# Kernel optimization log

Hardware: AMD Instinct MI355X
Metric: run time of the kernel (lower is better)

Reference implementation:

```python
import jax, jax.numpy as jnp
import numpy as np

B, S, D, NH, NKV, HD = 1, 2048, 4096, 32, 8, 128
SCALE = HD ** -0.5


def setup_inputs() -> dict:
    key = jax.random.key(0)
    ks = jax.random.split(key, 5)
    sd = D ** -0.5
    x = jax.random.normal(ks[0], (B, S, D), jnp.float32)
    Wq = jax.random.normal(ks[1], (D, NH * HD), jnp.float32) * sd
    Wk = jax.random.normal(ks[2], (D, NKV * HD), jnp.float32) * sd
    Wv = jax.random.normal(ks[3], (D, NKV * HD), jnp.float32) * sd
    Wo = jax.random.normal(ks[4], (NH * HD, D), jnp.float32) * sd
    # real rotary tables (rotate-half convention), shape [S, HD]
    inv_freq = 1.0 / (10000.0 ** (np.arange(0, HD, 2, dtype=np.float64) / HD))
    ang = np.outer(np.arange(S, dtype=np.float64), inv_freq)  # [S, HD//2]
    emb = np.concatenate([ang, ang], axis=-1)  # [S, HD]
    cos = jnp.asarray(np.cos(emb), jnp.float32)
    sin = jnp.asarray(np.sin(emb), jnp.float32)
    return dict(x=x, Wq=Wq, Wk=Wk, Wv=Wv, Wo=Wo, cos=cos, sin=sin)


def _rope(t, cos, sin):
    # t: [B,S,H,HD]; cos/sin: [S,HD]
    c = cos[None, :, None, :]
    s = sin[None, :, None, :]
    t1, t2 = jnp.split(t, 2, axis=-1)
    rot = jnp.concatenate([-t2, t1], axis=-1)
    return t * c + rot * s


def _to_i8(t):
    # per-vector absmax quantization over last dim
    scale = 127.0 / jnp.clip(jnp.max(jnp.abs(t), axis=-1, keepdims=True), 1e-5, None)
    q = jnp.clip(jnp.round(t * scale), -128.0, 127.0).astype(jnp.int8)
    return q, scale


def reference(x, Wq, Wk, Wv, Wo, cos, sin):
    q = (x @ Wq).reshape(B, S, NH, HD)
    k = (x @ Wk).reshape(B, S, NKV, HD)
    v = (x @ Wv).reshape(B, S, NKV, HD)
    q = _rope(q, cos, sin)
    k = _rope(k, cos, sin)
    q_i8, q_s = _to_i8(q)          # [B,S,NH,HD], [B,S,NH,1]
    k_i8, k_s = _to_i8(k)          # [B,S,NKV,HD], [B,S,NKV,1]
    rep = NH // NKV                # GQA expansion
    k_i8 = jnp.repeat(k_i8, rep, axis=2)
    k_s = jnp.repeat(k_s, rep, axis=2)
    v = jnp.repeat(v, rep, axis=2)
    # int8 QK^T accumulated in int32 (exact), then per-vector dequant
    scores = jnp.einsum('bshd,bthd->bhst', q_i8, k_i8,
                        preferred_element_type=jnp.int32).astype(jnp.float32)
    q_st = jnp.transpose(q_s, (0, 2, 1, 3))            # [B,NH,S,1]
    k_st = jnp.transpose(k_s, (0, 2, 3, 1))            # [B,NH,1,S]
    scores = scores * (SCALE / (q_st * k_st))
    # causal mask (seq > 1, no cache so total == S)
    mask = jnp.triu(jnp.full((S, S), -jnp.inf, jnp.float32), k=1)
    scores = scores + mask
    attn = jax.nn.softmax(scores, axis=-1)             # [B,NH,S,S]
    out = jnp.einsum('bhst,bthd->bshd', attn, v).reshape(B, S, NH * HD)
    return out @ Wo
```

## Files before the change

kernel.cpp:

```cpp
#include <hip/hip_runtime.h>
#include <hip/hip_bf16.h>

#define S_LEN 2048
#define DMODEL 4096
#define NH 32
#define NKV 8
#define HD 128
#define NQKV 6144
#define ATT_SCALE_L2E 0.1275175213528852f

typedef __bf16 bf16x8 __attribute__((ext_vector_type(8)));
typedef __bf16 bf16x4 __attribute__((ext_vector_type(4)));
typedef float f32x4 __attribute__((ext_vector_type(4)));

__device__ __forceinline__ unsigned short f2b(float f) {
  union { float f; unsigned u; } a; a.f = f;
  unsigned u = a.u;
  return (unsigned short)((u + 0x7FFFu + ((u >> 16) & 1u)) >> 16);
}
__device__ __forceinline__ float b2f(unsigned short u) {
  union { unsigned u; float f; } a; a.u = (unsigned)u << 16; return a.f;
}

__device__ __forceinline__ void gl16(const unsigned short* g, unsigned short* l) {
  __builtin_amdgcn_global_load_lds(
      (const __attribute__((address_space(1))) unsigned int*)g,
      (__attribute__((address_space(3))) unsigned int*)l, 16, 0, 0);
}

__global__ __launch_bounds__(256) void k_cvt_x(const float* __restrict__ x,
                                               unsigned short* __restrict__ xb) {
  int i = blockIdx.x * 256 + threadIdx.x;
  float4 v = ((const float4*)x)[i];
  ushort4 o;
  o.x = f2b(v.x); o.y = f2b(v.y); o.z = f2b(v.z); o.w = f2b(v.w);
  ((ushort4*)xb)[i] = o;
}

__global__ __launch_bounds__(256) void k_transpose(const float* __restrict__ W,
                                                   unsigned short* __restrict__ Wt,
                                                   int K, int N) {
  __shared__ float tile[64][65];
  int k0 = blockIdx.x * 64, n0 = blockIdx.y * 64;
  int tx = threadIdx.x & 31, ty = threadIdx.x >> 5;
#pragma unroll
  for (int i = 0; i < 8; ++i) {
    int k = ty + i * 8;
    const float* src = W + (size_t)(k0 + k) * N + n0;
    tile[k][tx] = src[tx];
    tile[k][tx + 32] = src[tx + 32];
  }
  __syncthreads();
  int kq = threadIdx.x & 15, nb = threadIdx.x >> 4;
#pragma unroll
  for (int i = 0; i < 4; ++i) {
    int n = nb + i * 16;
    ushort4 o;
    o.x = f2b(tile[kq * 4 + 0][n]);
    o.y = f2b(tile[kq * 4 + 1][n]);
    o.z = f2b(tile[kq * 4 + 2][n]);
    o.w = f2b(tile[kq * 4 + 3][n]);
    *(ushort4*)&Wt[(size_t)(n0 + n) * K + k0 + kq * 4] = o;
  }
}

__global__ __launch_bounds__(256) void k_vt(const unsigned short* __restrict__ v_bf,
                                            unsigned short* __restrict__ v_t) {
  __shared__ unsigned short tile[64][65];
  int s0 = blockIdx.x * 64, d0 = blockIdx.y * 64, kvh = blockIdx.z;
  int tx = threadIdx.x & 63, ty = threadIdx.x >> 6;
#pragma unroll
  for (int i = 0; i < 16; ++i) {
    int s = ty + i * 4;
    tile[s][tx] = v_bf[((size_t)(s0 + s) * NKV + kvh) * HD + d0 + tx];
  }
  __syncthreads();
#pragma unroll
  for (int i = 0; i < 16; ++i) {
    int d = ty + i * 4;
    v_t[((size_t)kvh * HD + d0 + d) * S_LEN + s0 + tx] = tile[tx][d];
  }
}

template <int FN, bool BF16OUT>
__global__ __launch_bounds__(512, 4) void k_g128(const unsigned short* __restrict__ A,
                                                 const unsigned short* __restrict__ B,
                                                 void* __restrict__ Cv,
                                                 int M, int N, int K) {
  extern __shared__ __align__(16) unsigned short smem[];
  char* Sc = (char*)smem;
  const int tid = threadIdx.x;
  const int wvid = tid >> 6, l = tid & 63;
  const int wm = wvid >> 2, wn = wvid & 3;
  const int l15 = l & 15, l4 = l >> 4;

  const int cpx = gridDim.x >> 3;
  const int swz = (blockIdx.x & 7) * cpx + (blockIdx.x >> 3);
  const int mtiles = M >> 7;
  const int m0 = (swz % mtiles) * 128;
  const int n0 = (swz / mtiles) * (FN * 64);

  const int NT = K >> 6;

  const int rsw = (l15 & 7) << 4;
  const int a_base = (wm * 64 + l15) * 128;
  const int b_base = (wn * FN * 16 + l15) * 128;
  const int c0 = (l4 * 16) ^ rsw;
  const int c1 = (64 + l4 * 16) ^ rsw;

  const int srow = l >> 3;
  const int st_k8 = (l & 7) ^ (srow & 7);

  auto stA = [&](int tt) {
    if (tt >= NT) return;
    const unsigned short* g = A + (size_t)(m0 + wvid * 8 + srow) * K + tt * 64 + st_k8 * 8;
    char* lb = Sc + (tt & 1) * 16384 + wvid * 1024;
#pragma unroll
    for (int j = 0; j < 2; ++j)
      gl16(g + (size_t)(j * 64) * K, (unsigned short*)(lb + j * 8192));
  };
  auto stB = [&](int tt) {
    if (tt >= NT) return;
    const unsigned short* g = B + (size_t)(n0 + wvid * 8 + srow) * K + tt * 64 + st_k8 * 8;
    char* lb = Sc + 32768 + (tt & 1) * (FN * 8192) + wvid * 1024;
#pragma unroll
    for (int j = 0; j < FN; ++j)
      gl16(g + (size_t)(j * 64) * K, (unsigned short*)(lb + j * 8192));
  };

  f32x4 acc[4][FN] = {};

  stA(0); stB(0); stA(1);
  if (NT > 1) asm volatile("s_waitcnt vmcnt(2)" ::: "memory");
  else        asm volatile("s_waitcnt vmcnt(0)" ::: "memory");
  __builtin_amdgcn_s_barrier();

  for (int t = 0; t < NT; ++t) {
    const char* Ab = Sc + (t & 1) * 16384;
    const char* Bb = Sc + 32768 + (t & 1) * (FN * 8192);
    stB(t + 1);
    bf16x8 a[4], b[FN];
#pragma unroll
    for (int fm = 0; fm < 4; ++fm) a[fm] = *(const bf16x8*)(Ab + a_base + fm * 2048 + c0);
#pragma unroll
    for (int fn = 0; fn < FN; ++fn) b[fn] = *(const bf16x8*)(Bb + b_base + fn * 2048 + c0);
    __builtin_amdgcn_s_setprio(1);
#pragma unroll
    for (int fm = 0; fm < 4; ++fm)
#pragma unroll
      for (int fn = 0; fn < FN; ++fn)
        acc[fm][fn] = __builtin_amdgcn_mfma_f32_16x16x32_bf16(a[fm], b[fn], acc[fm][fn], 0, 0, 0);
    __builtin_amdgcn_s_setprio(0);
#pragma unroll
    for (int fm = 0; fm < 4; ++fm) a[fm] = *(const bf16x8*)(Ab + a_base + fm * 2048 + c1);
#pragma unroll
    for (int fn = 0; fn < FN; ++fn) b[fn] = *(const bf16x8*)(Bb + b_base + fn * 2048 + c1);
    __builtin_amdgcn_s_setprio(1);
#pragma unroll
    for (int fm = 0; fm < 4; ++fm)
#pragma unroll
      for (int fn = 0; fn < FN; ++fn)
        acc[fm][fn] = __builtin_amdgcn_mfma_f32_16x16x32_bf16(a[fm], b[fn], acc[fm][fn], 0, 0, 0);
    __builtin_amdgcn_s_setprio(0);
    __builtin_amdgcn_s_barrier();
    stA(t + 2);
    if (t + 1 < NT) {
      if (t + 1 == NT - 1) asm volatile("s_waitcnt vmcnt(0)" ::: "memory");
      else                 asm volatile("s_waitcnt vmcnt(2)" ::: "memory");
      __builtin_amdgcn_s_barrier();
    }
  }

#pragma unroll
  for (int fm = 0; fm < 4; ++fm) {
    int row0 = m0 + wm * 64 + fm * 16 + l4 * 4;
#pragma unroll
    for (int fn = 0; fn < FN; ++fn) {
      int col = n0 + wn * FN * 16 + fn * 16 + l15;
#pragma unroll
      for (int r = 0; r < 4; ++r) {
        if constexpr (BF16OUT)
          ((unsigned short*)Cv)[(size_t)(row0 + r) * N + col] = f2b(acc[fm][fn][r]);
        else
          ((float*)Cv)[(size_t)(row0 + r) * N + col] = acc[fm][fn][r];
      }
    }
  }
}

__global__ __launch_bounds__(256) void k_ropequant(const unsigned short* __restrict__ qkv,
                                                   const float* __restrict__ cost,
                                                   const float* __restrict__ sint,
                                                   unsigned short* __restrict__ q_int,
                                                   float* __restrict__ q_ds_t,
                                                   unsigned short* __restrict__ k_int,
                                                   float* __restrict__ k_ds_t,
                                                   unsigned short* __restrict__ v_bf) {
  int s = blockIdx.x;
  int wv = threadIdx.x >> 6, l = threadIdx.x & 63;
  int hh = blockIdx.y * 4 + wv;
  const unsigned short* row = qkv + (size_t)s * NQKV;
  if (hh < NH + NKV) {
    int off = (hh < NH) ? hh * HD : DMODEL + (hh - NH) * HD;
    float t1 = b2f(row[off + l]), t2 = b2f(row[off + 64 + l]);
    float c1 = cost[s * HD + l],      sn1 = sint[s * HD + l];
    float c2 = cost[s * HD + 64 + l], sn2 = sint[s * HD + 64 + l];
    float o1 = t1 * c1 - t2 * sn1;
    float o2 = t2 * c2 + t1 * sn2;
    float amax = fmaxf(fabsf(o1), fabsf(o2));
#pragma unroll
    for (int m = 1; m < 64; m <<= 1) amax = fmaxf(amax, __shfl_xor(amax, m));
    amax = fmaxf(amax, 1e-5f);
    float scale = 127.0f / amax;
    float dscale = amax * (1.0f / 127.0f);
    float v1 = fminf(fmaxf(rintf(o1 * scale), -128.f), 127.f);
    float v2 = fminf(fmaxf(rintf(o2 * scale), -128.f), 127.f);
    if (hh < NH) {
      unsigned short* dst = q_int + ((size_t)s * NH + hh) * HD;
      dst[l] = f2b(v1); dst[l + 64] = f2b(v2);
      if (l == 0) q_ds_t[(size_t)hh * S_LEN + s] = dscale;
    } else {
      int kh = hh - NH;
      unsigned short* dst = k_int + ((size_t)s * NKV + kh) * HD;
      dst[l] = f2b(v1); dst[l + 64] = f2b(v2);
      if (l == 0) k_ds_t[(size_t)kh * S_LEN + s] = dscale;
    }
  } else {
    int vh = hh - (NH + NKV);
    const unsigned short* src = row + DMODEL + NKV * HD + vh * HD;
    unsigned short* dst = v_bf + ((size_t)s * NKV + vh) * HD;
    dst[l] = src[l];
    dst[l + 64] = src[l + 64];
  }
}

__global__ __launch_bounds__(256) void k_attn(const unsigned short* __restrict__ q_int,
                                              const float* __restrict__ q_ds_t,
                                              const unsigned short* __restrict__ k_int,
                                              const float* __restrict__ k_ds_t,
                                              const unsigned short* __restrict__ v_t,
                                              unsigned short* __restrict__ o_bf) {
  __shared__ __align__(16) unsigned short K_lds[2][8192];
  __shared__ __align__(16) unsigned short V_lds[2][8192];
  __shared__ __align__(16) unsigned short P_lds[4][16 * 72];

  const int bid = blockIdx.x;
  const int kvh = bid & 7;
  const int ha = kvh * 4 + ((bid >> 3) & 1) * 2;
  const int qt = 31 - (bid >> 4);
  const int tid = threadIdx.x, wv = tid >> 6, l = tid & 63;
  const int l15 = l & 15, l4 = l >> 4;

  auto stage = [&](int b, int kt) {
    const unsigned short* kB = k_int + (size_t)kt * 64 * (NKV * HD) + kvh * HD;
    const unsigned short* vB = v_t + (size_t)kvh * HD * S_LEN + (size_t)kt * 64;
#pragma unroll
    for (int j = 0; j < 4; ++j) {
      int wi = j * 4 + wv;
      int slot = wi * 64 + l;
      int key = slot >> 4;
      int colb = ((slot & 15) * 16) ^ ((key & 7) << 4);
      gl16(kB + key * (NKV * HD) + (colb >> 1), &K_lds[b][wi * 512]);
      int d = slot >> 3;
      int ckb = ((slot & 7) * 16) ^ ((d & 7) << 4);
      gl16(vB + (size_t)d * S_LEN + (ckb >> 1), &V_lds[b][wi * 512]);
    }
  };

  const int qrow_lo = qt * 64 + wv * 16;
  const int qg = qrow_lo + l15;
  const int crow = qrow_lo + l4 * 4;

  bf16x8 qf[2][4];
  float qsS[2];
#pragma unroll
  for (int h2 = 0; h2 < 2; ++h2) {
    const unsigned short* qp = q_int + ((size_t)(qrow_lo + l15) * NH + ha + h2) * HD + l4 * 8;
#pragma unroll
    for (int kd = 0; kd < 4; ++kd) qf[h2][kd] = *(const bf16x8*)(qp + kd * 32);
    qsS[h2] = ATT_SCALE_L2E * q_ds_t[(size_t)(ha + h2) * S_LEN + qg];
  }

  float m_run[2] = {-3.0e38f, -3.0e38f};
  float l_run[2] = {0.f, 0.f};
  f32x4 o_acc[2][8] = {};

  const int nkt = qt + 1;
  stage(0, 0);
  __syncthreads();

  for (int kt = 0; kt < nkt; ++kt) {
    const int cur = kt & 1;
    f32x4 ksd[4];
    {
      const f32x4* kdp = (const f32x4*)(k_ds_t + (size_t)kvh * S_LEN + kt * 64 + l4 * 4);
#pragma unroll
      for (int nt = 0; nt < 4; ++nt) ksd[nt] = kdp[nt * 4];
    }
    if (kt + 1 < nkt) stage(cur ^ 1, kt + 1);

    f32x4 sacc[2][4] = {};
#pragma unroll
    for (int nt = 0; nt < 4; ++nt) {
      int key = nt * 16 + l15;
#pragma unroll
      for (int kd = 0; kd < 4; ++kd) {
        int byte = key * 256 + kd * 64 + l4 * 16;
        byte ^= (key & 7) << 4;
        bf16x8 kf = *(const bf16x8*)((const char*)&K_lds[cur][0] + byte);
        sacc[0][nt] = __builtin_amdgcn_mfma_f32_16x16x32_bf16(kf, qf[0][kd], sacc[0][nt], 0, 0, 0);
        sacc[1][nt] = __builtin_amdgcn_mfma_f32_16x16x32_bf16(kf, qf[1][kd], sacc[1][nt], 0, 0, 0);
      }
    }

    bf16x8 pa[2][2];
#pragma unroll
    for (int h2 = 0; h2 < 2; ++h2) {
      float p[4][4];
      float tmax = -3.0e38f;
#pragma unroll
      for (int nt = 0; nt < 4; ++nt) {
        int keyb = kt * 64 + nt * 16 + l4 * 4;
#pragma unroll
        for (int r = 0; r < 4; ++r) {
          float sc = sacc[h2][nt][r] * (qsS[h2] * ksd[nt][r]);
          sc = (keyb + r <= qg) ? sc : -3.0e38f;
          p[nt][r] = sc;
          tmax = fmaxf(tmax, sc);
        }
      }
      tmax = fmaxf(tmax, __shfl_xor(tmax, 16));
      tmax = fmaxf(tmax, __shfl_xor(tmax, 32));

      float nm = fmaxf(m_run[h2], tmax);
      bool need = tmax > m_run[h2] + 11.0f;
      if (__ballot(need)) {
        float corr = __builtin_amdgcn_exp2f(m_run[h2] - nm);
        m_run[h2] = nm;
        l_run[h2] *= corr;
        float cq[4];
#pragma unroll
        for (int r = 0; r < 4; ++r) cq[r] = __shfl(corr, (l & 48) | (l4 * 4 + r));
#pragma unroll
        for (int dt = 0; dt < 8; ++dt)
#pragma unroll
          for (int r = 0; r < 4; ++r) o_acc[h2][dt][r] *= cq[r];
      }

      float psum = 0.f;
#pragma unroll
      for (int nt = 0; nt < 4; ++nt)
#pragma unroll
        for (int r = 0; r < 4; ++r) {
          float e = __builtin_amdgcn_exp2f(p[nt][r] - m_run[h2]);
          p[nt][r] = e;
          psum += e;
        }
      psum += __shfl_xor(psum, 16);
      psum += __shfl_xor(psum, 32);
      l_run[h2] += psum;

#pragma unroll
      for (int nt = 0; nt < 4; ++nt) {
        bf16x4 pk;
        pk[0] = (__bf16)p[nt][0]; pk[1] = (__bf16)p[nt][1];
        pk[2] = (__bf16)p[nt][2]; pk[3] = (__bf16)p[nt][3];
        *(bf16x4*)((char*)&P_lds[wv][0] + l15 * 144 + nt * 32 + l4 * 8) = pk;
      }
#pragma unroll
      for (int kc = 0; kc < 2; ++kc)
        pa[h2][kc] = *(const bf16x8*)((const char*)&P_lds[wv][0] + l15 * 144 + kc * 64 + l4 * 16);
    }

#pragma unroll
    for (int dt = 0; dt < 8; ++dt) {
      int d = dt * 16 + l15;
      int swzv = (d & 7) << 4;
#pragma unroll
      for (int kc = 0; kc < 2; ++kc) {
        int byte = d * 128 + ((kc * 64 + l4 * 16) ^ swzv);
        bf16x8 vb = *(const bf16x8*)((const char*)&V_lds[cur][0] + byte);
        o_acc[0][dt] = __builtin_amdgcn_mfma_f32_16x16x32_bf16(pa[0][kc], vb, o_acc[0][dt], 0, 0, 0);
        o_acc[1][dt] = __builtin_amdgcn_mfma_f32_16x16x32_bf16(pa[1][kc], vb, o_acc[1][dt], 0, 0, 0);
      }
    }
    __syncthreads();
  }

#pragma unroll
  for (int h2 = 0; h2 < 2; ++h2) {
    float inv = 1.0f / l_run[h2];
    float invq[4];
#pragma unroll
    for (int r = 0; r < 4; ++r) invq[r] = __shfl(inv, (l & 48) | (l4 * 4 + r));
#pragma unroll
    for (int dt = 0; dt < 8; ++dt)
#pragma unroll
      for (int r = 0; r < 4; ++r)
        o_bf[(size_t)(crow + r) * (NH * HD) + (ha + h2) * HD + dt * 16 + l15] =
            f2b(o_acc[h2][dt][r] * invq[r]);
  }
}

extern "C" void kernel_launch(void* const* d_in, const int* in_sizes, int n_in,
                              void* d_out, int out_size, void* d_ws, size_t ws_size,
                              hipStream_t stream) {
  const float* x    = (const float*)d_in[0];
  const float* Wq   = (const float*)d_in[1];
  const float* Wk   = (const float*)d_in[2];
  const float* Wv   = (const float*)d_in[3];
  const float* Wo   = (const float*)d_in[4];
  const float* cost = (const float*)d_in[5];
  const float* sint = (const float*)d_in[6];
  float* out = (float*)d_out;
  char* ws = (char*)d_ws;

  unsigned short* xb     = (unsigned short*)(ws);
  unsigned short* wqkv_t = (unsigned short*)(ws + 16777216);
  unsigned short* wo_t   = (unsigned short*)(ws + 67108864);
  unsigned short* qkv    = (unsigned short*)(ws + 100663296);
  unsigned short* q_int  = (unsigned short*)(ws + 150994944);
  unsigned short* k_int  = (unsigned short*)(ws + 167772160);
  unsigned short* v_bf   = (unsigned short*)(ws + 171966464);
  float*          q_ds_t = (float*)(ws + 176160768);
  float*          k_ds_t = (float*)(ws + 176422912);
  unsigned short* o_bf   = (unsigned short*)(ws + 176488448);
  unsigned short* v_t    = (unsigned short*)(ws);

  hipFuncSetAttribute((const void*)k_g128<3, true>,
                      hipFuncAttributeMaxDynamicSharedMemorySize, 81920);
  hipFuncSetAttribute((const void*)k_g128<2, false>,
                      hipFuncAttributeMaxDynamicSharedMemorySize, 65536);

  k_cvt_x<<<(S_LEN * DMODEL / 4) / 256, 256, 0, stream>>>(x, xb);
  k_transpose<<<dim3(64, 64), 256, 0, stream>>>(Wq, wqkv_t, 4096, 4096);
  k_transpose<<<dim3(64, 16), 256, 0, stream>>>(Wk, wqkv_t + (size_t)4096 * 4096, 4096, 1024);
  k_transpose<<<dim3(64, 16), 256, 0, stream>>>(Wv, wqkv_t + (size_t)5120 * 4096, 4096, 1024);
  k_transpose<<<dim3(64, 64), 256, 0, stream>>>(Wo, wo_t, 4096, 4096);
  k_g128<3, true><<<dim3(512), 512, 81920, stream>>>(xb, wqkv_t, qkv, 2048, 6144, 4096);
  k_ropequant<<<dim3(2048, 12), 256, 0, stream>>>(qkv, cost, sint, q_int, q_ds_t, k_int, k_ds_t, v_bf);
  k_vt<<<dim3(32, 2, 8), 256, 0, stream>>>(v_bf, v_t);
  k_attn<<<dim3(512), 256, 0, stream>>>(q_int, q_ds_t, k_int, k_ds_t, v_t, o_bf);
  k_g128<2, false><<<dim3(512), 512, 65536, stream>>>(o_bf, wo_t, out, 2048, 4096, 4096);
}
```

Before: 330.6 us.

## Switch GEMM kernel to 32x32x16 MFMA with 4 waves per block

Rewrites the bf16 GEMM inner loop to use 32x32x16 MFMA instructions instead of 16x16x32. Blocks drop from 8 to 4 waves, so each wave computes a larger 64x(TN*32) sub-tile. The staging loops and waitcnt values change to match the larger per-wave load share. The aim is fewer LDS reads per FLOP and better MFMA efficiency, at the cost of more accumulator registers per wave and fewer waves to hide latency.

```diff
diff --git a/kernel.cpp b/kernel.cpp
--- a/kernel.cpp
+++ b/kernel.cpp
@@ -12,6 +12,7 @@
 typedef __bf16 bf16x8 __attribute__((ext_vector_type(8)));
 typedef __bf16 bf16x4 __attribute__((ext_vector_type(4)));
 typedef float f32x4 __attribute__((ext_vector_type(4)));
+typedef float f32x16 __attribute__((ext_vector_type(16)));
 
 __device__ __forceinline__ unsigned short f2b(float f) {
   union { float f; unsigned u; } a; a.f = f;
@@ -82,8 +83,8 @@
   }
 }
 
-template <int FN, bool BF16OUT>
-__global__ __launch_bounds__(512, 4) void k_g128(const unsigned short* __restrict__ A,
+template <int TN, bool BF16OUT>
+__global__ __launch_bounds__(256, 2) void k_g128(const unsigned short* __restrict__ A,
                                                  const unsigned short* __restrict__ B,
                                                  void* __restrict__ Cv,
                                                  int M, int N, int K) {
@@ -91,99 +92,98 @@
   char* Sc = (char*)smem;
   const int tid = threadIdx.x;
   const int wvid = tid >> 6, l = tid & 63;
-  const int wm = wvid >> 2, wn = wvid & 3;
-  const int l15 = l & 15, l4 = l >> 4;
+  const int wm = wvid >> 1, wn = wvid & 1;
+  const int l31 = l & 31, lh = l >> 5;
 
   const int cpx = gridDim.x >> 3;
   const int swz = (blockIdx.x & 7) * cpx + (blockIdx.x >> 3);
   const int mtiles = M >> 7;
   const int m0 = (swz % mtiles) * 128;
-  const int n0 = (swz / mtiles) * (FN * 64);
+  const int n0 = (swz / mtiles) * (TN * 64);
 
   const int NT = K >> 6;
 
-  const int rsw = (l15 & 7) << 4;
-  const int a_base = (wm * 64 + l15) * 128;
-  const int b_base = (wn * FN * 16 + l15) * 128;
-  const int c0 = (l4 * 16) ^ rsw;
-  const int c1 = (64 + l4 * 16) ^ rsw;
+  const int rsw = (l & 7) << 4;
+  const int a_row = (wm * 64 + l31) * 128;
+  const int b_row = (wn * TN * 32 + l31) * 128;
 
   const int srow = l >> 3;
   const int st_k8 = (l & 7) ^ (srow & 7);
 
   auto stA = [&](int tt) {
     if (tt >= NT) return;
-    const unsigned short* g = A + (size_t)(m0 + wvid * 8 + srow) * K + tt * 64 + st_k8 * 8;
-    char* lb = Sc + (tt & 1) * 16384 + wvid * 1024;
-#pragma unroll
-    for (int j = 0; j < 2; ++j)
-      gl16(g + (size_t)(j * 64) * K, (unsigned short*)(lb + j * 8192));
+    unsigned short* lb = (unsigned short*)(Sc + (tt & 1) * 16384);
+#pragma unroll
+    for (int j = 0; j < 4; ++j) {
+      int c = j * 4 + wvid;
+      gl16(A + (size_t)(m0 + c * 8 + srow) * K + tt * 64 + st_k8 * 8, lb + c * 512);
+    }
   };
   auto stB = [&](int tt) {
     if (tt >= NT) return;
-    const unsigned short* g = B + (size_t)(n0 + wvid * 8 + srow) * K + tt * 64 + st_k8 * 8;
-    char* lb = Sc + 32768 + (tt & 1) * (FN * 8192) + wvid * 1024;
-#pragma unroll
-    for (int j = 0; j < FN; ++j)
-      gl16(g + (size_t)(j * 64) * K, (unsigned short*)(lb + j * 8192));
+    unsigned short* lb = (unsigned short*)(Sc + 32768 + (tt & 1) * (TN * 8192));
+#pragma unroll
+    for (int j = 0; j < TN * 2; ++j) {
+      int c = j * 4 + wvid;
+      gl16(B + (size_t)(n0 + c * 8 + srow) * K + tt * 64 + st_k8 * 8, lb + c * 512);
+    }
   };
 
-  f32x4 acc[4][FN] = {};
+  f32x16 acc[2][TN] = {};
 
   stA(0); stB(0); stA(1);
-  if (NT > 1) asm volatile("s_waitcnt vmcnt(2)" ::: "memory");
+  if (NT > 1) asm volatile("s_waitcnt vmcnt(4)" ::: "memory");
   else        asm volatile("s_waitcnt vmcnt(0)" ::: "memory");
   __builtin_amdgcn_s_barrier();
 
   for (int t = 0; t < NT; ++t) {
     const char* Ab = Sc + (t & 1) * 16384;
-    const char* Bb = Sc + 32768 + (t & 1) * (FN * 8192);
+    const char* Bb = Sc + 32768 + (t & 1) * (TN * 8192);
     stB(t + 1);
-    bf16x8 a[4], b[FN];
-#pragma unroll
-    for (int fm = 0; fm < 4; ++fm) a[fm] = *(const bf16x8*)(Ab + a_base + fm * 2048 + c0);
-#pragma unroll
-    for (int fn = 0; fn < FN; ++fn) b[fn] = *(const bf16x8*)(Bb + b_base + fn * 2048 + c0);
-    __builtin_amdgcn_s_setprio(1);
-#pragma unroll
-    for (int fm = 0; fm < 4; ++fm)
-#pragma unroll
-      for (int fn = 0; fn < FN; ++fn)
-        acc[fm][fn] = __builtin_amdgcn_mfma_f32_16x16x32_bf16(a[fm], b[fn], acc[fm][fn], 0, 0, 0);
-    __builtin_amdgcn_s_setprio(0);
-#pragma unroll
-    for (int fm = 0; fm < 4; ++fm) a[fm] = *(const bf16x8*)(Ab + a_base + fm * 2048 + c1);
-#pragma unroll
-    for (int fn = 0; fn < FN; ++fn) b[fn] = *(const bf16x8*)(Bb + b_base + fn * 2048 + c1);
-    __builtin_amdgcn_s_setprio(1);
-#pragma unroll
-    for (int fm = 0; fm < 4; ++fm)
-#pragma unroll
-      for (int fn = 0; fn < FN; ++fn)
-        acc[fm][fn] = __builtin_amdgcn_mfma_f32_16x16x32_bf16(a[fm], b[fn], acc[fm][fn], 0, 0, 0);
-    __builtin_amdgcn_s_setprio(0);
+#pragma unroll
+    for (int ks = 0; ks < 4; ++ks) {
+      const int col = ((ks * 32 + lh * 16)) ^ rsw;
+      bf16x8 a[2], b[TN];
+#pragma unroll
+      for (int tm = 0; tm < 2; ++tm)
+        a[tm] = *(const bf16x8*)(Ab + a_row + tm * 4096 + col);
+#pragma unroll
+      for (int tn = 0; tn < TN; ++tn)
+        b[tn] = *(const bf16x8*)(Bb + b_row + tn * 4096 + col);
+      __builtin_amdgcn_s_setprio(1);
+#pragma unroll
+      for (int tm = 0; tm < 2; ++tm)
+#pragma unroll
+        for (int tn = 0; tn < TN; ++tn)
+          acc[tm][tn] = __builtin_amdgcn_mfma_f32_32x32x16_bf16(a[tm], b[tn], acc[tm][tn], 0, 0, 0);
+      __builtin_amdgcn_s_setprio(0);
+    }
     __builtin_amdgcn_s_barrier();
     stA(t + 2);
     if (t + 1 < NT) {
       if (t + 1 == NT - 1) asm volatile("s_waitcnt vmcnt(0)" ::: "memory");
-      else                 asm volatile("s_waitcnt vmcnt(2)" ::: "memory");
+      else                 asm volatile("s_waitcnt vmcnt(4)" ::: "memory");
       __builtin_amdgcn_s_barrier();
     }
   }
 
 #pragma unroll
-  for (int fm = 0; fm < 4; ++fm) {
-    int row0 = m0 + wm * 64 + fm * 16 + l4 * 4;
-#pragma unroll
-    for (int fn = 0; fn < FN; ++fn) {
-      int col = n0 + wn * FN * 16 + fn * 16 + l15;
-#pragma unroll
-      for (int r = 0; r < 4; ++r) {
-        if constexpr (BF16OUT)
-          ((unsigned short*)Cv)[(size_t)(row0 + r) * N + col] = f2b(acc[fm][fn][r]);
-        else
-          ((float*)Cv)[(size_t)(row0 + r) * N + col] = acc[fm][fn][r];
-      }
+  for (int tm = 0; tm < 2; ++tm) {
+    int rowb = m0 + wm * 64 + tm * 32 + 4 * lh;
+#pragma unroll
+    for (int tn = 0; tn < TN; ++tn) {
+      int col = n0 + wn * TN * 32 + tn * 32 + l31;
+#pragma unroll
+      for (int rg = 0; rg < 4; ++rg)
+#pragma unroll
+        for (int rr = 0; rr < 4; ++rr) {
+          int row = rowb + rg * 8 + rr;
+          float v = acc[tm][tn][rg * 4 + rr];
+          if constexpr (BF16OUT)
+            ((unsigned short*)Cv)[(size_t)row * N + col] = f2b(v);
+          else
+            ((float*)Cv)[(size_t)row * N + col] = v;
+        }
     }
   }
 }
@@ -437,9 +437,9 @@
   k_transpose<<<dim3(64, 16), 256, 0, stream>>>(Wk, wqkv_t + (size_t)4096 * 4096, 4096, 1024);
   k_transpose<<<dim3(64, 16), 256, 0, stream>>>(Wv, wqkv_t + (size_t)5120 * 4096, 4096, 1024);
   k_transpose<<<dim3(64, 64), 256, 0, stream>>>(Wo, wo_t, 4096, 4096);
-  k_g128<3, true><<<dim3(512), 512, 81920, stream>>>(xb, wqkv_t, qkv, 2048, 6144, 4096);
+  k_g128<3, true><<<dim3(512), 256, 81920, stream>>>(xb, wqkv_t, qkv, 2048, 6144, 4096);
   k_ropequant<<<dim3(2048, 12), 256, 0, stream>>>(qkv, cost, sint, q_int, q_ds_t, k_int, k_ds_t, v_bf);
   k_vt<<<dim3(32, 2, 8), 256, 0, stream>>>(v_bf, v_t);
   k_attn<<<dim3(512), 256, 0, stream>>>(q_int, q_ds_t, k_int, k_ds_t, v_t, o_bf);
-  k_g128<2, false><<<dim3(512), 512, 65536, stream>>>(o_bf, wo_t, out, 2048, 4096, 4096);
-}
+  k_g128<2, false><<<dim3(512), 256, 65536, stream>>>(o_bf, wo_t, out, 2048, 4096, 4096);
+}
```

New measurement: 351.2 us. 1.06x slower.

## Remap attention blocks to cover all four GQA heads per KV tile

Applied to the files above, without the earlier changes.

The attention kernel moves from 256 threads handling 2 query heads × 64 rows per block to 512 threads (8 waves), where each wave handles one of the 4 heads sharing a KV head for 16 of 32 rows. Each staged K/V tile is now reused by all four grouped heads instead of two. The causal tiling becomes finer (32-row query tiles), which trims wasted work on diagonal tiles. The P scratch buffer also gets an XOR swizzle to reduce LDS bank conflicts. In exchange, per-wave MFMA work per tile is halved and the larger blocks may lower occupancy or change register pressure.

```diff
diff --git a/kernel.cpp b/kernel.cpp
--- a/kernel.cpp
+++ b/kernel.cpp
@@ -234,29 +234,30 @@
   }
 }
 
-__global__ __launch_bounds__(256) void k_attn(const unsigned short* __restrict__ q_int,
-                                              const float* __restrict__ q_ds_t,
-                                              const unsigned short* __restrict__ k_int,
-                                              const float* __restrict__ k_ds_t,
-                                              const unsigned short* __restrict__ v_t,
-                                              unsigned short* __restrict__ o_bf) {
+__global__ __launch_bounds__(512, 4) void k_attn(const unsigned short* __restrict__ q_int,
+                                                 const float* __restrict__ q_ds_t,
+                                                 const unsigned short* __restrict__ k_int,
+                                                 const float* __restrict__ k_ds_t,
+                                                 const unsigned short* __restrict__ v_t,
+                                                 unsigned short* __restrict__ o_bf) {
   __shared__ __align__(16) unsigned short K_lds[2][8192];
   __shared__ __align__(16) unsigned short V_lds[2][8192];
-  __shared__ __align__(16) unsigned short P_lds[4][16 * 72];
+  __shared__ __align__(16) unsigned short P_lds[8][1024];
 
   const int bid = blockIdx.x;
   const int kvh = bid & 7;
-  const int ha = kvh * 4 + ((bid >> 3) & 1) * 2;
-  const int qt = 31 - (bid >> 4);
+  const int qt = 63 - (bid >> 3);
   const int tid = threadIdx.x, wv = tid >> 6, l = tid & 63;
   const int l15 = l & 15, l4 = l >> 4;
+  const int h = kvh * 4 + (wv & 3);
+  const int rh = wv >> 2;
 
   auto stage = [&](int b, int kt) {
     const unsigned short* kB = k_int + (size_t)kt * 64 * (NKV * HD) + kvh * HD;
     const unsigned short* vB = v_t + (size_t)kvh * HD * S_LEN + (size_t)kt * 64;
 #pragma unroll
-    for (int j = 0; j < 4; ++j) {
-      int wi = j * 4 + wv;
+    for (int j = 0; j < 2; ++j) {
+      int wi = j * 8 + wv;
       int slot = wi * 64 + l;
       int key = slot >> 4;
       int colb = ((slot & 15) * 16) ^ ((key & 7) << 4);
@@ -267,28 +268,26 @@
     }
   };
 
-  const int qrow_lo = qt * 64 + wv * 16;
+  const int qrow_lo = qt * 32 + rh * 16;
   const int qg = qrow_lo + l15;
   const int crow = qrow_lo + l4 * 4;
 
-  bf16x8 qf[2][4];
-  float qsS[2];
-#pragma unroll
-  for (int h2 = 0; h2 < 2; ++h2) {
-    const unsigned short* qp = q_int + ((size_t)(qrow_lo + l15) * NH + ha + h2) * HD + l4 * 8;
-#pragma unroll
-    for (int kd = 0; kd < 4; ++kd) qf[h2][kd] = *(const bf16x8*)(qp + kd * 32);
-    qsS[h2] = ATT_SCALE_L2E * q_ds_t[(size_t)(ha + h2) * S_LEN + qg];
-  }
-
-  float m_run[2] = {-3.0e38f, -3.0e38f};
-  float l_run[2] = {0.f, 0.f};
-  f32x4 o_acc[2][8] = {};
-
-  const int nkt = qt + 1;
+  bf16x8 qf[4];
+  {
+    const unsigned short* qp = q_int + ((size_t)qg * NH + h) * HD + l4 * 8;
+#pragma unroll
+    for (int kd = 0; kd < 4; ++kd) qf[kd] = *(const bf16x8*)(qp + kd * 32);
+  }
+  const float qsS = ATT_SCALE_L2E * q_ds_t[(size_t)h * S_LEN + qg];
+
+  float m_run = -3.0e38f, l_run = 0.f;
+  f32x4 o_acc[8] = {};
+
+  const int nkt = (qt >> 1) + 1;
   stage(0, 0);
   __syncthreads();
 
+  const int psw = (l15 & 7) << 4;
   for (int kt = 0; kt < nkt; ++kt) {
     const int cur = kt & 1;
     f32x4 ksd[4];
@@ -299,7 +298,7 @@
     }
     if (kt + 1 < nkt) stage(cur ^ 1, kt + 1);
 
-    f32x4 sacc[2][4] = {};
+    f32x4 sacc[4] = {};
 #pragma unroll
     for (int nt = 0; nt < 4; ++nt) {
       int key = nt * 16 + l15;
@@ -308,68 +307,67 @@
         int byte = key * 256 + kd * 64 + l4 * 16;
         byte ^= (key & 7) << 4;
         bf16x8 kf = *(const bf16x8*)((const char*)&K_lds[cur][0] + byte);
-        sacc[0][nt] = __builtin_amdgcn_mfma_f32_16x16x32_bf16(kf, qf[0][kd], sacc[0][nt], 0, 0, 0);
-        sacc[1][nt] = __builtin_amdgcn_mfma_f32_16x16x32_bf16(kf, qf[1][kd], sacc[1][nt], 0, 0, 0);
+        sacc[nt] = __builtin_amdgcn_mfma_f32_16x16x32_bf16(kf, qf[kd], sacc[nt], 0, 0, 0);
       }
     }
 
-    bf16x8 pa[2][2];
-#pragma unroll
-    for (int h2 = 0; h2 < 2; ++h2) {
-      float p[4][4];
-      float tmax = -3.0e38f;
-#pragma unroll
-      for (int nt = 0; nt < 4; ++nt) {
-        int keyb = kt * 64 + nt * 16 + l4 * 4;
-#pragma unroll
-        for (int r = 0; r < 4; ++r) {
-          float sc = sacc[h2][nt][r] * (qsS[h2] * ksd[nt][r]);
-          sc = (keyb + r <= qg) ? sc : -3.0e38f;
-          p[nt][r] = sc;
-          tmax = fmaxf(tmax, sc);
-        }
+    float p[4][4];
+    float tmax = -3.0e38f;
+#pragma unroll
+    for (int nt = 0; nt < 4; ++nt) {
+      int keyb = kt * 64 + nt * 16 + l4 * 4;
+#pragma unroll
+      for (int r = 0; r < 4; ++r) {
+        float sc = sacc[nt][r] * (qsS * ksd[nt][r]);
+        sc = (keyb + r <= qg) ? sc : -3.0e38f;
+        p[nt][r] = sc;
+        tmax = fmaxf(tmax, sc);
       }
-      tmax = fmaxf(tmax, __shfl_xor(tmax, 16));
-      tmax = fmaxf(tmax, __shfl_xor(tmax, 32));
-
-      float nm = fmaxf(m_run[h2], tmax);
-      bool need = tmax > m_run[h2] + 11.0f;
-      if (__ballot(need)) {
-        float corr = __builtin_amdgcn_exp2f(m_run[h2] - nm);
-        m_run[h2] = nm;
-        l_run[h2] *= corr;
-        float cq[4];
-#pragma unroll
-        for (int r = 0; r < 4; ++r) cq[r] = __shfl(corr, (l & 48) | (l4 * 4 + r));
-#pragma unroll
-        for (int dt = 0; dt < 8; ++dt)
-#pragma unroll
-          for (int r = 0; r < 4; ++r) o_acc[h2][dt][r] *= cq[r];
+    }
+    tmax = fmaxf(tmax, __shfl_xor(tmax, 16));
+    tmax = fmaxf(tmax, __shfl_xor(tmax, 32));
+
+    float nm = fmaxf(m_run, tmax);
+    bool need = tmax > m_run + 11.0f;
+    if (__ballot(need)) {
+      float corr = __builtin_amdgcn_exp2f(m_run - nm);
+      m_run = nm;
+      l_run *= corr;
+      float cq[4];
+#pragma unroll
+      for (int r = 0; r < 4; ++r) cq[r] = __shfl(corr, (l & 48) | (l4 * 4 + r));
+#pragma unroll
+      for (int dt = 0; dt < 8; ++dt)
+#pragma unroll
+        for (int r = 0; r < 4; ++r) o_acc[dt][r] *= cq[r];
+    }
+
+    float psum = 0.f;
+#pragma unroll
+    for (int nt = 0; nt < 4; ++nt)
+#pragma unroll
+      for (int r = 0; r < 4; ++r) {
+        float e = __builtin_amdgcn_exp2f(p[nt][r] - m_run);
+        p[nt][r] = e;
+        psum += e;
       }
-
-      float psum = 0.f;
-#pragma unroll
-      for (int nt = 0; nt < 4; ++nt)
-#pragma unroll
-        for (int r = 0; r < 4; ++r) {
-          float e = __builtin_amdgcn_exp2f(p[nt][r] - m_run[h2]);
-          p[nt][r] = e;
-          psum += e;
-        }
-      psum += __shfl_xor(psum, 16);
-      psum += __shfl_xor(psum, 32);
-      l_run[h2] += psum;
-
-#pragma unroll
-      for (int nt = 0; nt < 4; ++nt) {
-        bf16x4 pk;
-        pk[0] = (__bf16)p[nt][0]; pk[1] = (__bf16)p[nt][1];
-        pk[2] = (__bf16)p[nt][2]; pk[3] = (__bf16)p[nt][3];
-        *(bf16x4*)((char*)&P_lds[wv][0] + l15 * 144 + nt * 32 + l4 * 8) = pk;
-      }
-#pragma unroll
-      for (int kc = 0; kc < 2; ++kc)
-        pa[h2][kc] = *(const bf16x8*)((const char*)&P_lds[wv][0] + l15 * 144 + kc * 64 + l4 * 16);
+    psum += __shfl_xor(psum, 16);
+    psum += __shfl_xor(psum, 32);
+    l_run += psum;
+
+#pragma unroll
+    for (int nt = 0; nt < 4; ++nt) {
+      bf16x4 pk;
+      pk[0] = (__bf16)p[nt][0]; pk[1] = (__bf16)p[nt][1];
+      pk[2] = (__bf16)p[nt][2]; pk[3] = (__bf16)p[nt][3];
+      int bw = l15 * 128 + ((nt * 32 + l4 * 8) ^ psw);
+      *(bf16x4*)((char*)&P_lds[wv][0] + bw) = pk;
+    }
+    bf16x8 pa[2];
+#pragma unroll
+    for (int kc = 0; kc < 2; ++kc) {
+      int br = l15 * 128 + ((kc * 64 + l4 * 16) ^ psw);
+      pa[kc] = *(const bf16x8*)((const char*)&P_lds[wv][0] + br);
     }
 
 #pragma unroll
@@ -380,26 +378,22 @@
       for (int kc = 0; kc < 2; ++kc) {
         int byte = d * 128 + ((kc * 64 + l4 * 16) ^ swzv);
         bf16x8 vb = *(const bf16x8*)((const char*)&V_lds[cur][0] + byte);
-        o_acc[0][dt] = __builtin_amdgcn_mfma_f32_16x16x32_bf16(pa[0][kc], vb, o_acc[0][dt], 0, 0, 0);
-        o_acc[1][dt] = __builtin_amdgcn_mfma_f32_16x16x32_bf16(pa[1][kc], vb, o_acc[1][dt], 0, 0, 0);
+        o_acc[dt] = __builtin_amdgcn_mfma_f32_16x16x32_bf16(pa[kc], vb, o_acc[dt], 0, 0, 0);
       }
     }
     __syncthreads();
   }
 
-#pragma unroll
-  for (int h2 = 0; h2 < 2; ++h2) {
-    float inv = 1.0f / l_run[h2];
-    float invq[4];
-#pragma unroll
-    for (int r = 0; r < 4; ++r) invq[r] = __shfl(inv, (l & 48) | (l4 * 4 + r));
-#pragma unroll
-    for (int dt = 0; dt < 8; ++dt)
-#pragma unroll
-      for (int r = 0; r < 4; ++r)
-        o_bf[(size_t)(crow + r) * (NH * HD) + (ha + h2) * HD + dt * 16 + l15] =
-            f2b(o_acc[h2][dt][r] * invq[r]);
-  }
+  float inv = 1.0f / l_run;
+  float invq[4];
+#pragma unroll
+  for (int r = 0; r < 4; ++r) invq[r] = __shfl(inv, (l & 48) | (l4 * 4 + r));
+#pragma unroll
+  for (int dt = 0; dt < 8; ++dt)
+#pragma unroll
+    for (int r = 0; r < 4; ++r)
+      o_bf[(size_t)(crow + r) * (NH * HD) + h * HD + dt * 16 + l15] =
+          f2b(o_acc[dt][r] * invq[r]);
 }
 
 extern "C" void kernel_launch(void* const* d_in, const int* in_sizes, int n_in,
@@ -440,6 +434,6 @@
   k_g128<3, true><<<dim3(512), 512, 81920, stream>>>(xb, wqkv_t, qkv, 2048, 6144, 4096);
   k_ropequant<<<dim3(2048, 12), 256, 0, stream>>>(qkv, cost, sint, q_int, q_ds_t, k_int, k_ds_t, v_bf);
   k_vt<<<dim3(32, 2, 8), 256, 0, stream>>>(v_bf, v_t);
-  k_attn<<<dim3(512), 256, 0, stream>>>(q_int, q_ds_t, k_int, k_ds_t, v_t, o_bf);
+  k_attn<<<dim3(512), 512, 0, stream>>>(q_int, q_ds_t, k_int, k_ds_t, v_t, o_bf);
   k_g128<2, false><<<dim3(512), 512, 65536, stream>>>(o_bf, wo_t, out, 2048, 4096, 4096);
 }
```

Result: no change. 330.1 us (-0.1%).
